# Kernel tuning notes

Measured on AMD Instinct MI355X. Metric: run time of the kernel, lower is better.

The kernel has to match this reference:

```python
import jax, jax.numpy as jnp
import numpy as np

H, D = 8, 16          # heads, per-head dim (hidden_channels=128)
HID = H * D
N = 200000            # movie nodes
E = 500000            # edges per metapath relation
IN = 256              # input feature dim
CLS = 3               # output classes


def setup_inputs() -> dict:
    key = jax.random.key(0)
    ks = jax.random.split(key, 13)
    return {
        "x_movie": jax.random.normal(ks[0], (N, IN), jnp.float32),
        "W_proj": jax.random.normal(ks[1], (IN, HID), jnp.float32) * 0.05,
        "b_proj": jnp.zeros((HID,), jnp.float32),
        "att_src0": jax.random.normal(ks[2], (H, D), jnp.float32) * 0.1,
        "att_dst0": jax.random.normal(ks[3], (H, D), jnp.float32) * 0.1,
        "att_src1": jax.random.normal(ks[4], (H, D), jnp.float32) * 0.1,
        "att_dst1": jax.random.normal(ks[5], (H, D), jnp.float32) * 0.1,
        "q": jax.random.normal(ks[6], (HID,), jnp.float32) * 0.1,
        "k_w": jax.random.normal(ks[7], (HID, HID), jnp.float32) * 0.05,
        "k_b": jnp.zeros((HID,), jnp.float32),
        "lin_w": jax.random.normal(ks[8], (HID, CLS), jnp.float32) * 0.05,
        "lin_b": jnp.zeros((CLS,), jnp.float32),
        "e0_src": jax.random.randint(ks[9], (E,), 0, N, jnp.int32),
        "e0_dst": jax.random.randint(ks[10], (E,), 0, N, jnp.int32),
        "e1_src": jax.random.randint(ks[11], (E,), 0, N, jnp.int32),
        "e1_dst": jax.random.randint(ks[12], (E,), 0, N, jnp.int32),
    }


def _han_rel(h, att_s, att_d, src, dst, n):
    # h: [N, H, D]; GAT-style per-relation attention with segment softmax over dst
    a_s = jnp.sum(h * att_s, axis=-1)                      # [N, H]
    a_d = jnp.sum(h * att_d, axis=-1)                      # [N, H]
    alpha = jax.nn.leaky_relu(a_s[src] + a_d[dst], 0.2)    # [E, H]
    m = jax.ops.segment_max(alpha, dst, num_segments=n)    # per-dst max
    ex = jnp.exp(alpha - m[dst])
    den = jax.ops.segment_sum(ex, dst, num_segments=n)
    w = ex / (den[dst] + 1e-16)                            # edge softmax (PyG eps)
    msg = (h[src] * w[:, :, None]).reshape(-1, HID)        # [E, HID]
    return jax.nn.relu(jax.ops.segment_sum(msg, dst, num_segments=n))


def reference(x_movie, W_proj, b_proj, att_src0, att_dst0, att_src1, att_dst1,
              q, k_w, k_b, lin_w, lin_b, e0_src, e0_dst, e1_src, e1_dst):
    # node-type projection (HANConv.proj), dropout omitted (eval mode)
    h = (x_movie @ W_proj + b_proj).reshape(-1, H, D)      # [N, H, D]
    out0 = _han_rel(h, att_src0, att_dst0, e0_src, e0_dst, N)  # [N, HID]
    out1 = _han_rel(h, att_src1, att_dst1, e1_src, e1_dst, N)
    # semantic-level attention (HANConv.group)
    outs = jnp.stack([out0, out1])                         # [M=2, N, HID]
    score = jnp.sum(jnp.tanh(outs @ k_w + k_b).mean(axis=1) * q, axis=-1)  # [M]
    beta = jax.nn.softmax(score)
    fused = jnp.einsum('m,mnf->nf', beta, outs)            # [N, HID]
    return fused @ lin_w + lin_b                           # [N, CLS]
```

## Files before the change

### kernel.cpp

```cpp
#include <hip/hip_runtime.h>


typedef __attribute__((ext_vector_type(8))) short bf16x8;
typedef __attribute__((ext_vector_type(4))) float f32x4;
typedef __attribute__((ext_vector_type(8))) unsigned short ushort8;

__device__ __forceinline__ unsigned short f2b(float f) {
  union { float f; unsigned u; } v; v.f = f;
  unsigned r = v.u + 0x7fffu + ((v.u >> 16) & 1u);
  return (unsigned short)(r >> 16);
}
__device__ __forceinline__ float b2f(unsigned short u) {
  union { unsigned u; float f; } v; v.u = ((unsigned)u) << 16;
  return v.f;
}
__device__ __forceinline__ float fast_tanh(float x) {
  x = fminf(fmaxf(x, -15.f), 15.f);
  float t = __expf(2.f * x);
  return 1.f - 2.f / (t + 1.f);
}
__device__ __forceinline__ void gload_lds16(const void* g, void* l) {
  __builtin_amdgcn_global_load_lds(
      (const __attribute__((address_space(1))) unsigned int*)g,
      (__attribute__((address_space(3))) unsigned int*)l, 16, 0, 0);
}

__global__ __launch_bounds__(256) void prep_lite(
    const int* __restrict__ e0d, const int* __restrict__ e1d,
    int* __restrict__ deg, int ne, int n,
    const float* __restrict__ Wp, const float* __restrict__ kwm,
    unsigned short* __restrict__ Wpf, unsigned short* __restrict__ Kwf) {
  const int tid = threadIdx.x;
  int b = blockIdx.x;
  const int cb = (2 * ne + 255) >> 8;
  if (b < cb) {
    int e = b * 256 + tid;
    if (e < ne) atomicAdd(&deg[e0d[e]], 1);
    else if (e < 2 * ne) atomicAdd(&deg[n + e1d[e - ne]], 1);
    return;
  }
  b -= cb;
  int t = b * 256 + tid;
  const float* W; unsigned short* Wf; int idx;
  if (t < 4096) { W = Wp; Wf = Wpf; idx = t; }
  else if (t < 6144) { W = kwm; Wf = Kwf; idx = t - 4096; }
  else return;
  int lane = idx & 63, nt = (idx >> 6) & 7, kt = idx >> 9;
  int c = lane & 15, ks = lane >> 4;
  int kbase = kt * 32 + ks * 8;
  int col = nt * 16 + c;
  ushort8 o;
#pragma unroll
  for (int j = 0; j < 8; ++j) o[j] = f2b(W[(size_t)(kbase + j) * 128 + col]);
  *(ushort8*)(Wf + (size_t)idx * 8) = o;
}

__global__ __launch_bounds__(256) void proj_mfma(
    const float* __restrict__ X, const unsigned short* __restrict__ Wf,
    const float* __restrict__ bias,
    const float* __restrict__ as0v, const float* __restrict__ ad0v,
    const float* __restrict__ as1v, const float* __restrict__ ad1v,
    unsigned short* __restrict__ Hb, float* __restrict__ preb, int n) {
  __shared__ float buf[2][4096];
  const int tid = threadIdx.x;
  const int wid = tid >> 6, lane = tid & 63;
  const int wm = wid >> 1, wn = wid & 1;
  const int row0 = blockIdx.x * 64;
  const int r = lane & 15, ks = lane >> 4;

  f32x4 acc[2][4] = {};
  const unsigned short* bptr = Wf + ((size_t)(wn * 4) * 64 + lane) * 8;
  bf16x8 Br0[8], Br1[8];

#define VMWAIT(N) asm volatile("s_waitcnt vmcnt(" #N ")" ::: "memory")
#define SBAR()                                                                 \
  {                                                                            \
    __builtin_amdgcn_sched_barrier(0);                                         \
    __builtin_amdgcn_s_barrier();                                              \
    __builtin_amdgcn_sched_barrier(0);                                         \
  }

#define STAGE(b, s)                                                            \
  {                                                                            \
    _Pragma("unroll")                                                          \
    for (int i = 0; i < 4; ++i) {                                              \
      int rloc = wid * 16 + i * 4 + ks;                                        \
      int grow = row0 + rloc;                                                  \
      grow = grow < n ? grow : n - 1;                                          \
      const float* src =                                                       \
          X + (size_t)grow * 256 + (s) * 64 + ((r ^ (rloc & 7)) << 2);         \
      gload_lds16(src, &buf[b][(wid * 16 + i * 4) * 64]);                      \
    }                                                                          \
  }

#define BLOAD(P, s)                                                            \
  {                                                                            \
    _Pragma("unroll")                                                          \
    for (int j = 0; j < 8; ++j)                                                \
      P[j] = *(const bf16x8*)(bptr +                                           \
                (((size_t)(s) * 2 + (j >> 2)) * 8 + (j & 3)) * 512);           \
  }

#define COMPUTE_R(b, P)                                                        \
  {                                                                            \
    _Pragma("unroll")                                                          \
    for (int kt = 0; kt < 2; ++kt) {                                           \
      bf16x8 a[2];                                                             \
      _Pragma("unroll")                                                        \
      for (int mi = 0; mi < 2; ++mi) {                                         \
        int rr = wm * 32 + mi * 16 + r;                                        \
        const float* lrow = &buf[b][rr * 64];                                  \
        int c0 = kt * 8 + ks * 2;                                              \
        int sw = rr & 7;                                                       \
        float4 f0 = *(const float4*)(lrow + ((c0 ^ sw) * 4));                  \
        float4 f1 = *(const float4*)(lrow + (((c0 + 1) ^ sw) * 4));            \
        bf16x8 v;                                                              \
        v[0] = (short)f2b(f0.x); v[1] = (short)f2b(f0.y);                      \
        v[2] = (short)f2b(f0.z); v[3] = (short)f2b(f0.w);                      \
        v[4] = (short)f2b(f1.x); v[5] = (short)f2b(f1.y);                      \
        v[6] = (short)f2b(f1.z); v[7] = (short)f2b(f1.w);                      \
        a[mi] = v;                                                             \
      }                                                                        \
      _Pragma("unroll")                                                        \
      for (int ni = 0; ni < 4; ++ni) {                                         \
        acc[0][ni] = __builtin_amdgcn_mfma_f32_16x16x32_bf16(                  \
            a[0], P[kt * 4 + ni], acc[0][ni], 0, 0, 0);                        \
        acc[1][ni] = __builtin_amdgcn_mfma_f32_16x16x32_bf16(                  \
            a[1], P[kt * 4 + ni], acc[1][ni], 0, 0, 0);                        \
      }                                                                        \
    }                                                                          \
  }

  STAGE(0, 0);
  BLOAD(Br0, 0);
  STAGE(1, 1);
  VMWAIT(4); SBAR();
  BLOAD(Br1, 1);
  COMPUTE_R(0, Br0);
  SBAR();
  STAGE(0, 2);
  VMWAIT(4); SBAR();
  BLOAD(Br0, 2);
  COMPUTE_R(1, Br1);
  SBAR();
  STAGE(1, 3);
  VMWAIT(4); SBAR();
  BLOAD(Br1, 3);
  COMPUTE_R(0, Br0);
  SBAR();
  VMWAIT(0); SBAR();
  COMPUTE_R(1, Br1);
  __syncthreads();
#undef STAGE
#undef BLOAD
#undef COMPUTE_R
#undef VMWAIT
#undef SBAR

  unsigned short* ct = (unsigned short*)&buf[0][0];
#pragma unroll
  for (int ni = 0; ni < 4; ++ni) {
    const int col = wn * 64 + ni * 16 + r;
    const float bv = bias[col];
#pragma unroll
    for (int mi = 0; mi < 2; ++mi)
#pragma unroll
      for (int i = 0; i < 4; ++i)
        ct[(wm * 32 + mi * 16 + ks * 4 + i) * 136 + col] = f2b(acc[mi][ni][i] + bv);
  }
  __syncthreads();

  {
    int row = tid >> 2, qq = tid & 3;
    int grow = row0 + row;
    if (grow < n) {
      ushort8* dst = (ushort8*)(Hb + (size_t)grow * 128 + qq * 32);
#pragma unroll
      for (int j = 0; j < 4; ++j) dst[j] = *(ushort8*)&ct[row * 136 + qq * 32 + j * 8];
    }
  }

  const size_t n8 = (size_t)n * 8;
  for (int rh = tid; rh < 512; rh += 256) {
    int row = rh >> 3, head = rh & 7;
    int node = row0 + row;
    if (node < n) {
      float hv[16];
#pragma unroll
      for (int j = 0; j < 16; ++j) hv[j] = b2f(ct[row * 136 + head * 16 + j]);
      float s0 = 0, d0 = 0, s1 = 0, d1 = 0;
      const float* p0 = as0v + head * 16;
      const float* p1 = ad0v + head * 16;
      const float* p2 = as1v + head * 16;
      const float* p3 = ad1v + head * 16;
#pragma unroll
      for (int j = 0; j < 16; ++j) {
        float v = hv[j];
        s0 += v * p0[j]; d0 += v * p1[j];
        s1 += v * p2[j]; d1 += v * p3[j];
      }
      size_t idx = (size_t)node * 8 + head;
      preb[idx] = s0;
      preb[n8 + idx] = d0;
      preb[2 * n8 + idx] = s1;
      preb[3 * n8 + idx] = d1;
    }
  }
}

__global__ __launch_bounds__(256) void scan1_kernel(
    const int* __restrict__ deg, int* __restrict__ pre, int* __restrict__ bsum, int m) {
  __shared__ int sd[256];
  int t = threadIdx.x;
  int base = blockIdx.x * 2048 + t * 8;
  int v[8], sum = 0;
#pragma unroll
  for (int j = 0; j < 8; ++j) {
    v[j] = (base + j < m) ? deg[base + j] : 0;
    sum += v[j];
  }
  sd[t] = sum;
  __syncthreads();
  for (int off = 1; off < 256; off <<= 1) {
    int x = (t >= off) ? sd[t - off] : 0;
    __syncthreads();
    if (t >= off) sd[t] += x;
    __syncthreads();
  }
  if (t == 255) bsum[blockIdx.x] = sd[255];
  int run = sd[t] - sum;
#pragma unroll
  for (int j = 0; j < 8; ++j) {
    if (base + j < m) pre[base + j] = run;
    run += v[j];
  }
}

__global__ __launch_bounds__(256) void scan2_kernel(int* __restrict__ bsum, int nb) {
  __shared__ int sd[256];
  int t = threadIdx.x;
  int v = (t < nb) ? bsum[t] : 0;
  sd[t] = v;
  __syncthreads();
  for (int off = 1; off < 256; off <<= 1) {
    int x = (t >= off) ? sd[t - off] : 0;
    __syncthreads();
    if (t >= off) sd[t] += x;
    __syncthreads();
  }
  if (t < nb) bsum[t] = sd[t] - v;
}

__global__ void scan3_kernel(int* __restrict__ pre, const int* __restrict__ bsum, int m, int total) {
  int i = blockIdx.x * 256 + threadIdx.x;
  if (i < m) pre[i] += bsum[i >> 11];
  if (i == m) pre[m] = total;
}

__global__ void fill2_kernel(const int* __restrict__ e0s, const int* __restrict__ e0d,
                             const int* __restrict__ e1s, const int* __restrict__ e1d,
                             const int* __restrict__ pre, int* __restrict__ cur,
                             int* __restrict__ csr, int ne, int n) {
  int e = blockIdx.x * 256 + threadIdx.x;
  int s, idx;
  if (e < ne) { idx = e0d[e]; s = e0s[e]; }
  else if (e < 2 * ne) { idx = n + e1d[e - ne]; s = e1s[e - ne]; }
  else return;
  int slot = pre[idx] + atomicAdd(&cur[idx], 1);
  csr[slot] = s;
}

__global__ __launch_bounds__(512) void aggscore_mfma(
    const int* __restrict__ pre, const int* __restrict__ csr,
    const unsigned short* __restrict__ Hb, const float* __restrict__ preb,
    const unsigned short* __restrict__ Kf, const float* __restrict__ kb,
    const float* __restrict__ q, const float* __restrict__ lw,
    float* __restrict__ pout, float* __restrict__ sb, int n) {
  __shared__ unsigned short at[16384];
  __shared__ float red[8];
  const int rel = blockIdx.y;
  const int tid = threadIdx.x;
  const int row0 = blockIdx.x * 128;
  const size_t n8 = (size_t)n * 8;
  const float* a_s = preb + (size_t)(2 * rel) * n8;
  const float* a_d = preb + (size_t)(2 * rel + 1) * n8;

  {
    const int lane8 = tid & 7;
    const int nsub = tid >> 3;
#pragma unroll
    for (int it = 0; it < 2; ++it) {
      int row = it * 64 + nsub;
      int node = row0 + row;
      float s = 0.f;
      float acc[16] = {};
      if (node < n) {
        int beg = pre[rel * n + node];
        int cnt = pre[rel * n + node + 1] - beg;
        if (cnt > 0) {
          float ad = a_d[(size_t)node * 8 + lane8];
          int i0 = csr[beg];
          int i1 = csr[beg + (cnt > 1 ? 1 : 0)];
          float as0 = a_s[(size_t)i0 * 8 + lane8];
          float as1 = a_s[(size_t)i1 * 8 + lane8];
          const ushort8* hp0 = (const ushort8*)(Hb + (size_t)i0 * 128 + lane8 * 16);
          const ushort8* hp1 = (const ushort8*)(Hb + (size_t)i1 * 128 + lane8 * 16);
          ushort8 h0a = hp0[0], h0b = hp0[1];
          ushort8 h1a = hp1[0], h1b = hp1[1];
          for (int k = 0; k < cnt; k += 2) {
            int c2 = (k + 2 < cnt) ? k + 2 : cnt - 1;
            int c3 = (k + 3 < cnt) ? k + 3 : cnt - 1;
            int j0 = csr[beg + c2], j1 = csr[beg + c3];
            float nas0 = a_s[(size_t)j0 * 8 + lane8];
            float nas1 = a_s[(size_t)j1 * 8 + lane8];
            const ushort8* np0 = (const ushort8*)(Hb + (size_t)j0 * 128 + lane8 * 16);
            const ushort8* np1 = (const ushort8*)(Hb + (size_t)j1 * 128 + lane8 * 16);
            ushort8 nh0a = np0[0], nh0b = np0[1];
            ushort8 nh1a = np1[0], nh1b = np1[1];
            float al0 = as0 + ad, al1 = as1 + ad;
            al0 = (al0 >= 0.f) ? al0 : 0.2f * al0;
            al1 = (al1 >= 0.f) ? al1 : 0.2f * al1;
            float p0 = __expf(al0);
            float p1 = (k + 1 < cnt) ? __expf(al1) : 0.f;
            s += p0 + p1;
#pragma unroll
            for (int j = 0; j < 8; ++j) {
              acc[j]     += p0 * b2f(h0a[j]) + p1 * b2f(h1a[j]);
              acc[8 + j] += p0 * b2f(h0b[j]) + p1 * b2f(h1b[j]);
            }
            as0 = nas0; as1 = nas1;
            h0a = nh0a; h0b = nh0b; h1a = nh1a; h1b = nh1b;
          }
        }
      }
      float inv = 1.f / (s + 1e-16f);
      ushort8 o0, o1;
#pragma unroll
      for (int j = 0; j < 8; ++j) {
        o0[j] = f2b(fmaxf(acc[j] * inv, 0.f));
        o1[j] = f2b(fmaxf(acc[8 + j] * inv, 0.f));
      }
      int sw = row & 7;
      *(ushort8*)&at[row * 128 + (((lane8 * 2) ^ sw) * 8)] = o0;
      *(ushort8*)&at[row * 128 + (((lane8 * 2 + 1) ^ sw) * 8)] = o1;
    }
  }
  __syncthreads();

  const int wid = tid >> 6;
  float part = 0.f;
  if (wid < 4) {
    const int lane = tid & 63;
    const int wm = wid >> 1, wn = wid & 1;
    const int r = lane & 15, ks = lane >> 4;
    f32x4 acc[4][4] = {};
    const unsigned short* bptr = Kf + ((size_t)(wn * 4) * 64 + lane) * 8;
#pragma unroll
    for (int kt = 0; kt < 4; ++kt) {
      bf16x8 a[4], b[4];
#pragma unroll
      for (int mi = 0; mi < 4; ++mi) {
        int row = wm * 64 + mi * 16 + r;
        a[mi] = *(const bf16x8*)&at[row * 128 + (((kt * 4 + ks) ^ (row & 7)) * 8)];
      }
#pragma unroll
      for (int ni = 0; ni < 4; ++ni)
        b[ni] = *(const bf16x8*)(bptr + ((size_t)kt * 8 + ni) * 512);
#pragma unroll
      for (int mi = 0; mi < 4; ++mi)
#pragma unroll
        for (int ni = 0; ni < 4; ++ni)
          acc[mi][ni] = __builtin_amdgcn_mfma_f32_16x16x32_bf16(a[mi], b[ni], acc[mi][ni], 0, 0, 0);
    }
#pragma unroll
    for (int ni = 0; ni < 4; ++ni) {
      const int col = wn * 64 + ni * 16 + r;
      const float kbv = kb[col], qv = q[col];
#pragma unroll
      for (int mi = 0; mi < 4; ++mi) {
#pragma unroll
        for (int i = 0; i < 4; ++i) {
          int row = row0 + wm * 64 + mi * 16 + ks * 4 + i;
          if (row < n) part += fast_tanh(acc[mi][ni][i] + kbv) * qv;
        }
      }
    }
  } else if (tid < 384) {
    int t2 = tid - 256;
    int node = row0 + t2;
    if (node < n) {
      float p0 = 0.f, p1 = 0.f, p2 = 0.f;
      int s = t2 & 7;
#pragma unroll
      for (int c = 0; c < 16; ++c) {
        const unsigned short* rp = &at[t2 * 128 + ((c ^ s) * 8)];
#pragma unroll
        for (int j = 0; j < 8; ++j) {
          float v = b2f(rp[j]);
          const float* w = lw + (size_t)(c * 8 + j) * 3;
          p0 += v * w[0]; p1 += v * w[1]; p2 += v * w[2];
        }
      }
      float4 o = make_float4(p0, p1, p2, 0.f);
      *(float4*)(pout + (size_t)node * 8 + rel * 4) = o;
    }
  }
#pragma unroll
  for (int off = 32; off > 0; off >>= 1) part += __shfl_down(part, off, 64);
  if ((tid & 63) == 0) red[wid] = part;
  __syncthreads();
  if (tid == 0) {
    float t = 0.f;
#pragma unroll
    for (int w = 0; w < 8; ++w) t += red[w];
    atomicAdd(&sb[rel], t);
  }
}

__global__ void beta_kernel(float* __restrict__ sb, float invn) {
  if (threadIdx.x == 0 && blockIdx.x == 0) {
    float s0 = sb[0] * invn, s1 = sb[1] * invn;
    float m = fmaxf(s0, s1);
    float e0 = __expf(s0 - m), e1 = __expf(s1 - m);
    float d = e0 + e1;
    sb[2] = e0 / d;
    sb[3] = e1 / d;
  }
}

__global__ __launch_bounds__(256) void final2_kernel(
    const float* __restrict__ pout, const float* __restrict__ sb,
    const float* __restrict__ lb, float* __restrict__ out, int n) {
  int node = blockIdx.x * 256 + threadIdx.x;
  if (node >= n) return;
  float b0 = sb[2], b1 = sb[3];
  const float4* p = (const float4*)(pout + (size_t)node * 8);
  float4 pa = p[0], pb = p[1];
  float* d = out + (size_t)node * 3;
  d[0] = b0 * pa.x + b1 * pb.x + lb[0];
  d[1] = b0 * pa.y + b1 * pb.y + lb[1];
  d[2] = b0 * pa.z + b1 * pb.z + lb[2];
}

extern "C" void kernel_launch(void* const* d_in, const int* in_sizes, int n_in,
                              void* d_out, int out_size, void* d_ws, size_t ws_size,
                              hipStream_t stream) {
  const float* x   = (const float*)d_in[0];
  const float* Wp  = (const float*)d_in[1];
  const float* bp  = (const float*)d_in[2];
  const float* as0 = (const float*)d_in[3];
  const float* ad0 = (const float*)d_in[4];
  const float* as1 = (const float*)d_in[5];
  const float* ad1 = (const float*)d_in[6];
  const float* q   = (const float*)d_in[7];
  const float* kw  = (const float*)d_in[8];
  const float* kb  = (const float*)d_in[9];
  const float* lw  = (const float*)d_in[10];
  const float* lb  = (const float*)d_in[11];
  const int* e0s = (const int*)d_in[12];
  const int* e0d = (const int*)d_in[13];
  const int* e1s = (const int*)d_in[14];
  const int* e1d = (const int*)d_in[15];
  const int n  = in_sizes[0] / 256;
  const int ne = in_sizes[12];
  float* out = (float*)d_out;

  char* ws = (char*)d_ws;
  size_t off = 0;
  auto alloc = [&](size_t b) -> char* {
    char* p = ws + off;
    off = (off + b + 255) & ~(size_t)255;
    return p;
  };
  unsigned short* h    = (unsigned short*)alloc((size_t)n * 128 * 2);
  float* preb = (float*)alloc((size_t)4 * n * 8 * 4);
  float* pout = (float*)alloc((size_t)n * 8 * 4);
  int* pre    = (int*)alloc((size_t)(2 * n + 1) * 4);
  int* csr    = (int*)alloc((size_t)2 * ne * 4);
  int* deg    = (int*)alloc(((size_t)4 * n + 4) * 4);
  int* cur    = deg + 2 * n;
  float* sb   = (float*)(deg + 4 * n);
  int* bsum   = (int*)alloc(256 * 4);
  unsigned short* Wpf = (unsigned short*)alloc((size_t)4096 * 8 * 2);
  unsigned short* Kwf = (unsigned short*)alloc((size_t)2048 * 8 * 2);

  const int m = 2 * n;
  const int nblk_scan = (m + 2047) / 2048;
  const int cnt_blks = (2 * ne + 255) / 256;

  hipMemsetAsync(deg, 0, ((size_t)4 * n + 4) * 4, stream);
  hipLaunchKernelGGL(prep_lite, dim3(cnt_blks + 24), dim3(256), 0, stream,
                     e0d, e1d, deg, ne, n, Wp, kw, Wpf, Kwf);

  const int gproj = (n + 63) / 64;
  hipLaunchKernelGGL(proj_mfma, dim3(gproj), dim3(256), 0, stream,
                     x, Wpf, bp, as0, ad0, as1, ad1, h, preb, n);

  hipLaunchKernelGGL(scan1_kernel, dim3(nblk_scan), dim3(256), 0, stream, deg, pre, bsum, m);
  hipLaunchKernelGGL(scan2_kernel, dim3(1), dim3(256), 0, stream, bsum, nblk_scan);
  hipLaunchKernelGGL(scan3_kernel, dim3((m + 1 + 255) / 256), dim3(256), 0, stream,
                     pre, bsum, m, 2 * ne);
  hipLaunchKernelGGL(fill2_kernel, dim3((2 * ne + 255) / 256), dim3(256), 0, stream,
                     e0s, e0d, e1s, e1d, pre, cur, csr, ne, n);

  hipLaunchKernelGGL(aggscore_mfma, dim3((n + 127) / 128, 2), dim3(512), 0, stream,
                     pre, csr, h, preb, Kwf, kb, q, lw, pout, sb, n);
  hipLaunchKernelGGL(beta_kernel, dim3(1), dim3(64), 0, stream, sb, 1.0f / n);
  hipLaunchKernelGGL(final2_kernel, dim3((n + 255) / 256), dim3(256), 0, stream,
                     pout, sb, lb, out, n);
}
```

Before: 297.0 us.

## Interleave degree counting into projection kernel and fold beta softmax into final kernel

Moves the atomic degree-counting blocks out of the weight-conversion kernel and into the projection GEMM launch. Projection and counting blocks are interleaved so the latency-bound atomics overlap with the compute- and bandwidth-bound projection tiles. The separate beta softmax kernel is removed; every thread of the final kernel now recomputes the two-way softmax, which costs one fewer launch but repeats the redundant math. It also raises wave priority around the MFMA loop in the score stage, and hardcodes the relation offset 200000 in the counting path.

```diff
diff --git a/kernel.cpp b/kernel.cpp
--- a/kernel.cpp
+++ b/kernel.cpp
@@ -25,22 +25,10 @@
       (__attribute__((address_space(3))) unsigned int*)l, 16, 0, 0);
 }
 
-__global__ __launch_bounds__(256) void prep_lite(
-    const int* __restrict__ e0d, const int* __restrict__ e1d,
-    int* __restrict__ deg, int ne, int n,
+__global__ __launch_bounds__(256) void wconv_kernel(
     const float* __restrict__ Wp, const float* __restrict__ kwm,
     unsigned short* __restrict__ Wpf, unsigned short* __restrict__ Kwf) {
-  const int tid = threadIdx.x;
-  int b = blockIdx.x;
-  const int cb = (2 * ne + 255) >> 8;
-  if (b < cb) {
-    int e = b * 256 + tid;
-    if (e < ne) atomicAdd(&deg[e0d[e]], 1);
-    else if (e < 2 * ne) atomicAdd(&deg[n + e1d[e - ne]], 1);
-    return;
-  }
-  b -= cb;
-  int t = b * 256 + tid;
+  int t = blockIdx.x * 256 + threadIdx.x;
   const float* W; unsigned short* Wf; int idx;
   if (t < 4096) { W = Wp; Wf = Wpf; idx = t; }
   else if (t < 6144) { W = kwm; Wf = Kwf; idx = t - 4096; }
@@ -55,17 +43,33 @@
   *(ushort8*)(Wf + (size_t)idx * 8) = o;
 }
 
-__global__ __launch_bounds__(256) void proj_mfma(
+__global__ __launch_bounds__(256) void projcnt_mfma(
     const float* __restrict__ X, const unsigned short* __restrict__ Wf,
     const float* __restrict__ bias,
     const float* __restrict__ as0v, const float* __restrict__ ad0v,
     const float* __restrict__ as1v, const float* __restrict__ ad1v,
-    unsigned short* __restrict__ Hb, float* __restrict__ preb, int n) {
+    unsigned short* __restrict__ Hb, float* __restrict__ preb,
+    const int* __restrict__ e0d, const int* __restrict__ e1d,
+    int* __restrict__ deg, int ne, int gproj, int cnt_blks, int n) {
   __shared__ float buf[2][4096];
   const int tid = threadIdx.x;
+
+  int b = blockIdx.x;
+  int small = gproj < cnt_blks ? gproj : cnt_blks;
+  int role, id;
+  if (b < 2 * small) { role = b & 1; id = b >> 1; }
+  else { id = b - 2 * small + small; role = (gproj < cnt_blks) ? 1 : 0; }
+
+  if (role == 1) {
+    int e = id * 256 + tid;
+    if (e < ne) atomicAdd(&deg[e0d[e]], 1);
+    else if (e < 2 * ne) atomicAdd(&deg[200000 + e1d[e - ne]], 1);
+    return;
+  }
+
   const int wid = tid >> 6, lane = tid & 63;
   const int wm = wid >> 1, wn = wid & 1;
-  const int row0 = blockIdx.x * 64;
+  const int row0 = id * 64;
   const int r = lane & 15, ks = lane >> 4;
 
   f32x4 acc[2][4] = {};
@@ -80,7 +84,7 @@
     __builtin_amdgcn_sched_barrier(0);                                         \
   }
 
-#define STAGE(b, s)                                                            \
+#define STAGE(bb, s)                                                           \
   {                                                                            \
     _Pragma("unroll")                                                          \
     for (int i = 0; i < 4; ++i) {                                              \
@@ -89,7 +93,7 @@
       grow = grow < n ? grow : n - 1;                                          \
       const float* src =                                                       \
           X + (size_t)grow * 256 + (s) * 64 + ((r ^ (rloc & 7)) << 2);         \
-      gload_lds16(src, &buf[b][(wid * 16 + i * 4) * 64]);                      \
+      gload_lds16(src, &buf[bb][(wid * 16 + i * 4) * 64]);                     \
     }                                                                          \
   }
 
@@ -101,7 +105,7 @@
                 (((size_t)(s) * 2 + (j >> 2)) * 8 + (j & 3)) * 512);           \
   }
 
-#define COMPUTE_R(b, P)                                                        \
+#define COMPUTE_R(bb, P)                                                       \
   {                                                                            \
     _Pragma("unroll")                                                          \
     for (int kt = 0; kt < 2; ++kt) {                                           \
@@ -109,7 +113,7 @@
       _Pragma("unroll")                                                        \
       for (int mi = 0; mi < 2; ++mi) {                                         \
         int rr = wm * 32 + mi * 16 + r;                                        \
-        const float* lrow = &buf[b][rr * 64];                                  \
+        const float* lrow = &buf[bb][rr * 64];                                 \
         int c0 = kt * 8 + ks * 2;                                              \
         int sw = rr & 7;                                                       \
         float4 f0 = *(const float4*)(lrow + ((c0 ^ sw) * 4));                  \
@@ -355,6 +359,7 @@
     const int r = lane & 15, ks = lane >> 4;
     f32x4 acc[4][4] = {};
     const unsigned short* bptr = Kf + ((size_t)(wn * 4) * 64 + lane) * 8;
+    __builtin_amdgcn_s_setprio(1);
 #pragma unroll
     for (int kt = 0; kt < 4; ++kt) {
       bf16x8 a[4], b[4];
@@ -372,6 +377,7 @@
         for (int ni = 0; ni < 4; ++ni)
           acc[mi][ni] = __builtin_amdgcn_mfma_f32_16x16x32_bf16(a[mi], b[ni], acc[mi][ni], 0, 0, 0);
     }
+    __builtin_amdgcn_s_setprio(0);
 #pragma unroll
     for (int ni = 0; ni < 4; ++ni) {
       const int col = wn * 64 + ni * 16 + r;
@@ -417,29 +423,22 @@
   }
 }
 
-__global__ void beta_kernel(float* __restrict__ sb, float invn) {
-  if (threadIdx.x == 0 && blockIdx.x == 0) {
-    float s0 = sb[0] * invn, s1 = sb[1] * invn;
-    float m = fmaxf(s0, s1);
-    float e0 = __expf(s0 - m), e1 = __expf(s1 - m);
-    float d = e0 + e1;
-    sb[2] = e0 / d;
-    sb[3] = e1 / d;
-  }
-}
-
-__global__ __launch_bounds__(256) void final2_kernel(
+__global__ __launch_bounds__(256) void final3_kernel(
     const float* __restrict__ pout, const float* __restrict__ sb,
-    const float* __restrict__ lb, float* __restrict__ out, int n) {
+    const float* __restrict__ lb, float* __restrict__ out, int n, float invn) {
   int node = blockIdx.x * 256 + threadIdx.x;
   if (node >= n) return;
-  float b0 = sb[2], b1 = sb[3];
+  float s0 = sb[0] * invn, s1 = sb[1] * invn;
+  float m = fmaxf(s0, s1);
+  float e0 = __expf(s0 - m), e1 = __expf(s1 - m);
+  float d = e0 + e1;
+  float b0 = e0 / d, b1 = e1 / d;
   const float4* p = (const float4*)(pout + (size_t)node * 8);
   float4 pa = p[0], pb = p[1];
-  float* d = out + (size_t)node * 3;
-  d[0] = b0 * pa.x + b1 * pb.x + lb[0];
-  d[1] = b0 * pa.y + b1 * pb.y + lb[1];
-  d[2] = b0 * pa.z + b1 * pb.z + lb[2];
+  float* dd = out + (size_t)node * 3;
+  dd[0] = b0 * pa.x + b1 * pb.x + lb[0];
+  dd[1] = b0 * pa.y + b1 * pb.y + lb[1];
+  dd[2] = b0 * pa.z + b1 * pb.z + lb[2];
 }
 
 extern "C" void kernel_launch(void* const* d_in, const int* in_sizes, int n_in,
@@ -486,15 +485,15 @@
 
   const int m = 2 * n;
   const int nblk_scan = (m + 2047) / 2048;
+  const int gproj = (n + 63) / 64;
   const int cnt_blks = (2 * ne + 255) / 256;
 
   hipMemsetAsync(deg, 0, ((size_t)4 * n + 4) * 4, stream);
-  hipLaunchKernelGGL(prep_lite, dim3(cnt_blks + 24), dim3(256), 0, stream,
-                     e0d, e1d, deg, ne, n, Wp, kw, Wpf, Kwf);
-
-  const int gproj = (n + 63) / 64;
-  hipLaunchKernelGGL(proj_mfma, dim3(gproj), dim3(256), 0, stream,
-                     x, Wpf, bp, as0, ad0, as1, ad1, h, preb, n);
+  hipLaunchKernelGGL(wconv_kernel, dim3(24), dim3(256), 0, stream, Wp, kw, Wpf, Kwf);
+
+  hipLaunchKernelGGL(projcnt_mfma, dim3(gproj + cnt_blks), dim3(256), 0, stream,
+                     x, Wpf, bp, as0, ad0, as1, ad1, h, preb,
+                     e0d, e1d, deg, ne, gproj, cnt_blks, n);
 
   hipLaunchKernelGGL(scan1_kernel, dim3(nblk_scan), dim3(256), 0, stream, deg, pre, bsum, m);
   hipLaunchKernelGGL(scan2_kernel, dim3(1), dim3(256), 0, stream, bsum, nblk_scan);
@@ -505,7 +504,6 @@
 
   hipLaunchKernelGGL(aggscore_mfma, dim3((n + 127) / 128, 2), dim3(512), 0, stream,
                      pre, csr, h, preb, Kwf, kb, q, lw, pout, sb, n);
-  hipLaunchKernelGGL(beta_kernel, dim3(1), dim3(64), 0, stream, sb, 1.0f / n);
-  hipLaunchKernelGGL(final2_kernel, dim3((n + 255) / 256), dim3(256), 0, stream,
-                     pout, sb, lb, out, n);
-}
+  hipLaunchKernelGGL(final3_kernel, dim3((n + 255) / 256), dim3(256), 0, stream,
+                     pout, sb, lb, out, n, 1.0f / n);
+}
```

After: 322.9 us. 1.09x slower.
